# Optimization experiments

Measured on AMD Instinct MI355X. Metric: run time of the kernel, lower is better.

## Reference

```python
import jax, jax.numpy as jnp
from jax import lax
import numpy as np

VGG_C = 512
INNER = 32


def _conv3x3(x, w, b):
    # x: [B,C,H,W], w: [O,I,3,3], padding=1 (SAME)
    y = lax.conv_general_dilated(x, w, (1, 1), 'SAME',
                                 dimension_numbers=('NCHW', 'OIHW', 'NCHW'))
    return y + b[None, :, None, None]


def _predict_filter(style, cw, cb, fw, fb):
    # FilterPredictor_S: conv 512->32, global mean pool, FC 32 -> 9*32*32
    s = _conv3x3(style, cw, cb)                     # [B,32,H,W]
    pooled = s.mean(axis=(2, 3))                    # [B,32]
    f = pooled @ fw.T + fb                          # [B,9216]
    return f.reshape(-1, INNER, INNER, 3, 3)        # [B,outC,inC,3,3]


def _apply_filter(x, filt):
    # per-sample dynamic 3x3 conv: x [B,32,H,W], filt [B,32,32,3,3]
    def one(xi, wi):
        return lax.conv_general_dilated(xi[None], wi, (1, 1), 'SAME',
                                        dimension_numbers=('NCHW', 'OIHW', 'NCHW'))[0]
    return jax.vmap(one)(x, filt)


def setup_inputs() -> dict:
    key = jax.random.key(0)
    ks = jax.random.split(key, 16)
    B, H, W = 8, 64, 64
    sc = 0.02
    d = {
        'content': jax.random.normal(ks[0], (B, VGG_C, H, W), jnp.float32),
        'style': jax.random.normal(ks[1], (B, VGG_C, H, W), jnp.float32),
        'ds_w': jax.random.normal(ks[2], (INNER, VGG_C, 3, 3), jnp.float32) * sc,
        'ds_b': jnp.zeros((INNER,), jnp.float32),
        'up_w': jax.random.normal(ks[3], (VGG_C, INNER, 3, 3), jnp.float32) * sc,
        'up_b': jnp.zeros((VGG_C,), jnp.float32),
        'f1_cw': jax.random.normal(ks[4], (INNER, VGG_C, 3, 3), jnp.float32) * sc,
        'f1_cb': jnp.zeros((INNER,), jnp.float32),
        'f1_fw': jax.random.normal(ks[5], (9 * INNER * INNER, INNER), jnp.float32) * sc,
        'f1_fb': jnp.zeros((9 * INNER * INNER,), jnp.float32),
        'f2_cw': jax.random.normal(ks[6], (INNER, VGG_C, 3, 3), jnp.float32) * sc,
        'f2_cb': jnp.zeros((INNER,), jnp.float32),
        'f2_fw': jax.random.normal(ks[7], (9 * INNER * INNER, INNER), jnp.float32) * sc,
        'f2_fb': jnp.zeros((9 * INNER * INNER,), jnp.float32),
    }
    return d


def reference(content, style, ds_w, ds_b, up_w, up_b,
              f1_cw, f1_cb, f1_fw, f1_fb,
              f2_cw, f2_cb, f2_fw, f2_fb):
    c = _conv3x3(content, ds_w, ds_b)                       # [B,32,H,W]
    filt1 = _predict_filter(style, f1_cw, f1_cb, f1_fw, f1_fb)
    c = _apply_filter(c, filt1)
    c = jnp.where(c >= 0, c, 0.2 * c)                       # LeakyReLU(0.2)
    filt2 = _predict_filter(style, f2_cw, f2_cb, f2_fw, f2_fb)
    c = _apply_filter(c, filt2)
    return content + _conv3x3(c, up_w, up_b)
```

## Files before the change

kernel.cpp:

```cpp
#include <hip/hip_runtime.h>
#include <hip/hip_bf16.h>

#define NB 8
#define NC 512
#define HW 4096
#define INNER 32

typedef unsigned short u16;
typedef unsigned int u32;
typedef __attribute__((ext_vector_type(8))) short bf16x8;
typedef __attribute__((ext_vector_type(4))) float f32x4;

__device__ __forceinline__ float b2f(u16 u) {
    union { u32 a; float f; } z;
    z.a = ((u32)u) << 16;
    return z.f;
}

__device__ __forceinline__ u16 f2b(float v) {
    u32 x = __float_as_uint(v);
    return (u16)((x + 0x7fffu + ((x >> 16) & 1u)) >> 16);
}

__device__ __forceinline__ float ldin(const void* p, int idx, int isf32) {
    if (isf32) return ((const float*)p)[idx];
    return b2f(((const u16*)p)[idx]);
}

__device__ __forceinline__ void gld_lds16(const void* g, void* l) {
    __builtin_amdgcn_global_load_lds(
        (const __attribute__((address_space(1))) unsigned int*)g,
        (__attribute__((address_space(3))) unsigned int*)l, 16, 0, 0);
}

__device__ __forceinline__ int resolve_isf32(int hisf, const void* content) {
    if (hisf >= 0) return hisf;
    int lane = threadIdx.x & 63;
    u16 u = ((const u16*)content)[lane * 2048];
    int e = (u >> 7) & 0xff;
    unsigned long long m = __ballot(e >= 100 && e <= 150);
    return (__popcll(m) < 32) ? 1 : 0;
}


__device__ __forceinline__ void role_style(int bc, const void* style,
        const void* cw1, const void* cw2, float* pooled_raw,
        int isf32, float* smf) {
    int b = bc >> 9, c = bc & 511;
    int base = bc * HW;
    int tid = threadIdx.x;
    float t = 0.f, top = 0.f, bot = 0.f, lft = 0.f, rgt = 0.f;
    if (isf32) {
        const float4* sp = (const float4*)((const float*)style + base);
#pragma unroll
        for (int k = 0; k < 4; k++) {
            int q = tid + k * 256;
            float4 v = sp[q];
            float s4 = (v.x + v.y) + (v.z + v.w);
            int h = q >> 4, w0 = (q & 15) * 4;
            t += s4;
            if (h == 0)   top += s4;
            if (h == 63)  bot += s4;
            if (w0 == 0)  lft += v.x;
            if (w0 == 60) rgt += v.w;
        }
    } else {
        const uint4* sp = (const uint4*)((const u16*)style + base);
#pragma unroll
        for (int k = 0; k < 2; k++) {
            int q = tid + k * 256;
            uint4 v = sp[q];
            float e0 = b2f((u16)(v.x & 0xffffu)), e1 = b2f((u16)(v.x >> 16));
            float e2 = b2f((u16)(v.y & 0xffffu)), e3 = b2f((u16)(v.y >> 16));
            float e4 = b2f((u16)(v.z & 0xffffu)), e5 = b2f((u16)(v.z >> 16));
            float e6 = b2f((u16)(v.w & 0xffffu)), e7 = b2f((u16)(v.w >> 16));
            float s8 = ((e0 + e1) + (e2 + e3)) + ((e4 + e5) + (e6 + e7));
            int h = q >> 3, w0 = (q & 7) * 8;
            t += s8;
            if (h == 0)   top += s8;
            if (h == 63)  bot += s8;
            if (w0 == 0)  lft += e0;
            if (w0 == 56) rgt += e7;
        }
    }
#pragma unroll
    for (int off = 32; off > 0; off >>= 1) {
        t   += __shfl_down(t, off);
        top += __shfl_down(top, off);
        bot += __shfl_down(bot, off);
        lft += __shfl_down(lft, off);
        rgt += __shfl_down(rgt, off);
    }
    int wave = tid >> 6;
    if ((tid & 63) == 0) {
        smf[20 + wave * 5 + 0] = t;   smf[20 + wave * 5 + 1] = top;
        smf[20 + wave * 5 + 2] = bot; smf[20 + wave * 5 + 3] = lft;
        smf[20 + wave * 5 + 4] = rgt;
    }
    __syncthreads();
    if (tid == 0) {
        t   = smf[20] + smf[25] + smf[30] + smf[35];
        top = smf[21] + smf[26] + smf[31] + smf[36];
        bot = smf[22] + smf[27] + smf[32] + smf[37];
        lft = smf[23] + smf[28] + smf[33] + smf[38];
        rgt = smf[24] + smf[29] + smf[34] + smf[39];
        float c00 = ldin(style, base + 0,    isf32);
        float c0W = ldin(style, base + 63,   isf32);
        float cH0 = ldin(style, base + 4032, isf32);
        float cHW = ldin(style, base + 4095, isf32);
        smf[0] = t - bot - rgt + cHW;
        smf[1] = t - bot;
        smf[2] = t - bot - lft + cH0;
        smf[3] = t - rgt;
        smf[4] = t;
        smf[5] = t - lft;
        smf[6] = t - top - rgt + c0W;
        smf[7] = t - top;
        smf[8] = t - top - lft + c00;
    }
    __syncthreads();
    if (tid < 64) {
        int set = tid >> 5, o = tid & 31;
        const void* cw = set ? cw2 : cw1;
        int wb = (o * NC + c) * 9;
        float acc = 0.f;
#pragma unroll
        for (int k = 0; k < 9; k++) acc += ldin(cw, wb + k, isf32) * smf[k];
        atomicAdd(&pooled_raw[(set * NB + b) * 32 + o], acc);
    }
}

__device__ __forceinline__ void role_transform(int ridx, const void* content,
        u16* cT, int bstart, int isf32, float* lds) {
    int hp = ridx & 31;
    int ci = (ridx >> 5) & 15;
    int b4 = ridx >> 9;
    int tid = threadIdx.x;
    size_t gbase = ((size_t)(bstart + b4) * NC + ci * 32) * HW + (size_t)hp * 128;
    if (isf32) {
#pragma unroll
        for (int r2 = 0; r2 < 2; r2++)
#pragma unroll
            for (int k = 0; k < 2; k++) {
                int q = tid + k * 256;
                int c = q >> 4, w0 = (q & 15) * 4;
                float4 v = *(const float4*)((const float*)content
                            + gbase + (size_t)c * HW + r2 * 64 + w0);
                float* dst = lds + r2 * 2080 + c * 65 + w0;
                dst[0] = v.x; dst[1] = v.y; dst[2] = v.z; dst[3] = v.w;
            }
    } else {
#pragma unroll
        for (int r2 = 0; r2 < 2; r2++) {
            int c = tid >> 3, w0 = (tid & 7) * 8;
            uint4 v = *(const uint4*)((const u16*)content
                        + gbase + (size_t)c * HW + r2 * 64 + w0);
            float* dst = lds + r2 * 2080 + c * 65 + w0;
            dst[0] = b2f((u16)(v.x & 0xffffu));
            dst[1] = b2f((u16)(v.x >> 16));
            dst[2] = b2f((u16)(v.y & 0xffffu));
            dst[3] = b2f((u16)(v.y >> 16));
            dst[4] = b2f((u16)(v.z & 0xffffu));
            dst[5] = b2f((u16)(v.z >> 16));
            dst[6] = b2f((u16)(v.w & 0xffffu));
            dst[7] = b2f((u16)(v.w >> 16));
        }
    }
    __syncthreads();
#pragma unroll
    for (int r2 = 0; r2 < 2; r2++) {
        u32* out = (u32*)(cT + ((size_t)(b4 * 16 + ci) * 4096
                                + (hp * 2 + r2) * 64) * 32);
        const float* src = lds + r2 * 2080;
#pragma unroll
        for (int k = 0; k < 4; k++) {
            int j = tid + k * 256;
            int w = j >> 4, cpair = j & 15;
            int key = (w + 1) & 3;
            int p0 = cpair << 1;
            int lc = (((p0 >> 3) ^ key) << 3) | (p0 & 7);
            out[j] = (u32)f2b(src[lc * 65 + w])
                   | ((u32)f2b(src[(lc + 1) * 65 + w]) << 16);
        }
    }
}

__device__ __forceinline__ void role_prep_wdown(int ridx, const void* dsw,
        u16* Bp, int isf32) {
    int idx = ridx * 256 + threadIdx.x;
    int e = idx & 7, l = (idx >> 3) & 63, nf = (idx >> 9) & 1;
    int cb = (idx >> 10) & 15, t9 = idx >> 14;
    int oc = nf * 16 + (l & 15);
    int c = cb * 32 + (l >> 4) * 8 + e;
    Bp[idx] = f2b(ldin(dsw, (oc * NC + c) * 9 + t9, isf32));
}

__device__ __forceinline__ void role_prep_wup(int ridx, const void* upw,
        u16* B2p, int isf32) {
    int idx = ridx * 256 + threadIdx.x;
    int e = idx & 7, l = (idx >> 3) & 63, nfo = (idx >> 9) & 31, t9 = idx >> 14;
    int oc = nfo * 16 + (l & 15);
    int ic = (l >> 4) * 8 + e;
    B2p[idx] = f2b(ldin(upw, (oc * INNER + ic) * 9 + t9, isf32));
}

__device__ __forceinline__ void role_fc(int ridx, const float* pooled_raw,
        const void* cbf1, const void* cbf2,
        const void* fw1, const void* fb1, const void* fw2, const void* fb2,
        u16* fpack, int isf32, float* p) {
    int set = ridx / 288;
    int rr = ridx - set * 288;
    int b = rr / 36;
    int chunk = rr - b * 36;
    int row = chunk * 256 + threadIdx.x;
    const void* fw = set ? fw2 : fw1;
    const void* fb = set ? fb2 : fb1;
    if (threadIdx.x < 32)
        p[threadIdx.x] = pooled_raw[(set * NB + b) * 32 + threadIdx.x]
                           * (1.0f / 4096.0f)
                       + ldin(set ? cbf2 : cbf1, threadIdx.x, isf32);
    __syncthreads();
    float acc = ldin(fb, row, isf32);
    if (isf32) {
        const float* fwf = (const float*)fw + row * 32;
#pragma unroll
        for (int j = 0; j < 32; j++) acc += fwf[j] * p[j];
    } else {
        const u32* w32 = (const u32*)((const u16*)fw + row * 32);
#pragma unroll
        for (int j = 0; j < 16; j++) {
            u32 u = w32[j];
            acc += b2f((u16)(u & 0xffffu)) * p[2 * j];
            acc += b2f((u16)(u >> 16)) * p[2 * j + 1];
        }
    }
    int oc = row / 288;
    int rem = row - oc * 288;
    int ic = rem / 9;
    int t9 = rem - ic * 9;
    int l = (oc & 15) | ((ic >> 3) << 4);
    int e = ic & 7;
    int nf = oc >> 4;
    fpack[((((set * NB + b) * 9 + t9) * 2 + nf) * 64 + l) * 8 + e] = f2b(acc);
}

__device__ __forceinline__ void role_conv_down(int x, const u16* cT,
        const u16* Bp, const void* dsb, u16* c0T, int bstart, int isf32,
        u16* lds) {
    u32* lds32 = (u32*)lds;
    int b4 = x >> 6, row = x & 63;
    int b = bstart + b4;
    int tid = threadIdx.x, lane = tid & 63;
    int wid = __builtin_amdgcn_readfirstlane(tid >> 6);
    for (int i = tid; i < 3 * 66 * 16; i += 256) lds32[i] = 0u;
    __syncthreads();

    int m = lane & 15, g = lane >> 4;
    int wbase = wid * 16;
    f32x4 acc0 = {0.f, 0.f, 0.f, 0.f}, acc1 = {0.f, 0.f, 0.f, 0.f};

    for (int ci = 0; ci < 16; ci++) {
        if (ci) __syncthreads();
        const u16* sp = cT + ((size_t)(b4 * 16 + ci) * 4096) * 32;
#pragma unroll
        for (int r = 0; r < 3; r++) {
            int gh = row + r - 1;
            if (gh >= 0 && gh < 64)
                gld_lds16(sp + (size_t)gh * 2048 + tid * 8,
                          (char*)lds + (r * 66 + 1) * 64 + wid * 1024);
        }
        __syncthreads();
#pragma unroll
        for (int t9 = 0; t9 < 9; t9++) {
            int dh = t9 / 3, dw = t9 - dh * 3;
            int wi = wbase + m + dw;
            bf16x8 a = *(const bf16x8*)(lds + ((dh * 66 + wi) * 32 + ((g ^ (wi & 3)) * 8)));
            bf16x8 b0 = ((const bf16x8*)Bp)[((t9 * 16 + ci) * 2 + 0) * 64 + lane];
            bf16x8 b1 = ((const bf16x8*)Bp)[((t9 * 16 + ci) * 2 + 1) * 64 + lane];
            acc0 = __builtin_amdgcn_mfma_f32_16x16x32_bf16(a, b0, acc0, 0, 0, 0);
            acc1 = __builtin_amdgcn_mfma_f32_16x16x32_bf16(a, b1, acc1, 0, 0, 0);
        }
    }
    float bia0 = ldin(dsb, m, isf32);
    float bia1 = ldin(dsb, 16 + m, isf32);
    size_t obase = ((size_t)b * 4096 + row * 64) * 32;
    int pix0 = wbase + g * 4;
#pragma unroll
    for (int r = 0; r < 4; r++) {
        int w = pix0 + r;
        int key = (w + 1) & 3;
        int p0 = (((m >> 3) ^ key) << 3) | (m & 7);
        int p1 = ((((16 + m) >> 3) ^ key) << 3) | (m & 7);
        c0T[obase + (size_t)w * 32 + p0] = f2b(acc0[r] + bia0);
        c0T[obase + (size_t)w * 32 + p1] = f2b(acc1[r] + bia1);
    }
}


__global__ __launch_bounds__(256) void k_front(
        const void* __restrict__ style,
        const void* __restrict__ cw1, const void* __restrict__ cw2,
        float* __restrict__ pooled_raw, int nStyle,
        const void* __restrict__ content, u16* __restrict__ cT, int bstart, int nT,
        const void* __restrict__ dsw, u16* __restrict__ Bp,
        const void* __restrict__ upw, u16* __restrict__ B2p, int nPrep,
        int hisf) {
    __shared__ float smf[2 * 2080];
    int isf32 = resolve_isf32(hisf, content);
    int x = blockIdx.x;
    if (x < nStyle) { role_style(x, style, cw1, cw2, pooled_raw, isf32, smf); return; }
    x -= nStyle;
    if (x < nT) { role_transform(x, content, cT, bstart, isf32, smf); return; }
    x -= nT;
    if (x < nPrep) { role_prep_wdown(x, dsw, Bp, isf32); return; }
    x -= nPrep;
    role_prep_wup(x, upw, B2p, isf32);
}

__global__ __launch_bounds__(256) void k_mid(
        const u16* __restrict__ cT, const u16* __restrict__ Bp,
        const void* __restrict__ dsb, u16* __restrict__ c0T, int bstart, int nCD,
        const float* __restrict__ pooled_raw,
        const void* __restrict__ cbf1, const void* __restrict__ cbf2,
        const void* __restrict__ fw1, const void* __restrict__ fb1,
        const void* __restrict__ fw2, const void* __restrict__ fb2,
        u16* __restrict__ fpack, const void* __restrict__ content, int hisf) {
    __shared__ u16 lds[3 * 66 * 32];
    int isf32 = resolve_isf32(hisf, content);
    int x = blockIdx.x;
    if (x < nCD) { role_conv_down(x, cT, Bp, dsb, c0T, bstart, isf32, lds); return; }
    role_fc(x - nCD, pooled_raw, cbf1, cbf2, fw1, fb1, fw2, fb2, fpack,
            isf32, (float*)lds);
}

__global__ __launch_bounds__(256) void k_apply(const u16* __restrict__ srcT,
        const u16* __restrict__ fpack, u16* __restrict__ dstT, int lrelu) {
    int b = blockIdx.x >> 6, row = blockIdx.x & 63;
    int tid = threadIdx.x, lane = tid & 63;
    int wid = __builtin_amdgcn_readfirstlane(tid >> 6);
    __shared__ u16 lds[3 * 66 * 32];
    u32* lds32 = (u32*)lds;
    for (int i = tid; i < 96; i += 256) {
        int r = i >> 5, side = (i >> 4) & 1, cpr = i & 15;
        lds32[(r * 66 + side * 65) * 16 + cpr] = 0u;
    }
    const u16* sp = srcT + (size_t)b * 64 * 64 * 32;
    for (int r = 0; r < 3; r++) {
        int gh = row + r - 1;
        u32 ldsoff = (u32)(r * 66 + 1) * 64 + (u32)wid * 1024;
        if (gh >= 0 && gh < 64) {
            gld_lds16(sp + (size_t)gh * 2048 + tid * 8, (char*)lds + ldsoff);
        } else {
            int4 z = make_int4(0, 0, 0, 0);
            *(int4*)((char*)lds + ldsoff + (u32)lane * 16) = z;
        }
    }
    __syncthreads();

    int m = lane & 15, g = lane >> 4, wbase = wid * 16;
    f32x4 acc0 = {0.f, 0.f, 0.f, 0.f}, acc1 = {0.f, 0.f, 0.f, 0.f};
    const bf16x8* FB = (const bf16x8*)fpack + (size_t)b * 1152;
#pragma unroll
    for (int t9 = 0; t9 < 9; t9++) {
        int dh = t9 / 3, dw = t9 - dh * 3;
        int wi = wbase + m + dw;
        bf16x8 a = *(const bf16x8*)(lds + ((dh * 66 + wi) * 32 + ((g ^ (wi & 3)) * 8)));
        bf16x8 b0 = FB[(t9 * 2 + 0) * 64 + lane];
        bf16x8 b1 = FB[(t9 * 2 + 1) * 64 + lane];
        acc0 = __builtin_amdgcn_mfma_f32_16x16x32_bf16(a, b0, acc0, 0, 0, 0);
        acc1 = __builtin_amdgcn_mfma_f32_16x16x32_bf16(a, b1, acc1, 0, 0, 0);
    }
    size_t obase = ((size_t)(b * 64 + row) * 64) * 32;
    int pix0 = wbase + g * 4;
#pragma unroll
    for (int r = 0; r < 4; r++) {
        float v0 = acc0[r], v1 = acc1[r];
        if (lrelu) {
            v0 = (v0 >= 0.f) ? v0 : 0.2f * v0;
            v1 = (v1 >= 0.f) ? v1 : 0.2f * v1;
        }
        int w = pix0 + r;
        int key = (w + 1) & 3;
        int p0 = (((m >> 3) ^ key) << 3) | (m & 7);
        int p1 = ((((16 + m) >> 3) ^ key) << 3) | (m & 7);
        dstT[obase + (size_t)w * 32 + p0] = f2b(v0);
        dstT[obase + (size_t)w * 32 + p1] = f2b(v1);
    }
}

__global__ __launch_bounds__(256) void k_conv_up(const u16* __restrict__ c2T,
        const u16* __restrict__ B2p, const void* __restrict__ upb,
        const void* __restrict__ content, void* __restrict__ outv, int hisf) {
    int isf32 = resolve_isf32(hisf, content);
    int b = blockIdx.x >> 6, row = blockIdx.x & 63;
    int nq = blockIdx.y;
    int tid = threadIdx.x, lane = tid & 63;
    int wid = __builtin_amdgcn_readfirstlane(tid >> 6);
    __shared__ char smem[64 * 68 * 4] __attribute__((aligned(16)));
    u16* lds = (u16*)smem;
    u32* lds32 = (u32*)smem;
    for (int i = tid; i < 96; i += 256) {
        int r = i >> 5, side = (i >> 4) & 1, cpr = i & 15;
        lds32[(r * 66 + side * 65) * 16 + cpr] = 0u;
    }
    const u16* sp = c2T + (size_t)b * 64 * 64 * 32;
    for (int r = 0; r < 3; r++) {
        int gh = row + r - 1;
        u32 ldsoff = (u32)(r * 66 + 1) * 64 + (u32)wid * 1024;
        if (gh >= 0 && gh < 64) {
            gld_lds16(sp + (size_t)gh * 2048 + tid * 8, (char*)lds + ldsoff);
        } else {
            int4 z = make_int4(0, 0, 0, 0);
            *(int4*)((char*)lds + ldsoff + (u32)lane * 16) = z;
        }
    }
    __syncthreads();

    int m = lane & 15, g = lane >> 4, wbase = wid * 16;
    f32x4 acc[8];
#pragma unroll
    for (int i = 0; i < 8; i++) acc[i] = (f32x4){0.f, 0.f, 0.f, 0.f};
#pragma unroll
    for (int t9 = 0; t9 < 9; t9++) {
        int dh = t9 / 3, dw = t9 - dh * 3;
        int wi = wbase + m + dw;
        bf16x8 a = *(const bf16x8*)(lds + ((dh * 66 + wi) * 32 + ((g ^ (wi & 3)) * 8)));
#pragma unroll
        for (int nfl = 0; nfl < 8; nfl++) {
            bf16x8 bw = ((const bf16x8*)B2p)[(t9 * 32 + nq * 8 + nfl) * 64 + lane];
            acc[nfl] = __builtin_amdgcn_mfma_f32_16x16x32_bf16(a, bw, acc[nfl], 0, 0, 0);
        }
    }

    int pix0 = wbase + g * 4;
    float* fl = (float*)smem;
    int ocl2 = tid >> 4;
    int px0 = (tid & 15) * 4;
    __syncthreads();
#pragma unroll
    for (int hf = 0; hf < 2; hf++) {
        if (hf) __syncthreads();
#pragma unroll
        for (int nf = 0; nf < 4; nf++) {
            int ocl = nf * 16 + m;
            *(f32x4*)(fl + ocl * 68 + pix0) = acc[hf * 4 + nf];
        }
        __syncthreads();
#pragma unroll
        for (int p = 0; p < 4; p++) {
            int ocl = p * 16 + ocl2;
            int oc = nq * 128 + hf * 64 + ocl;
            float bias = ldin(upb, oc, isf32);
            f32x4 v4 = *(const f32x4*)(fl + ocl * 68 + px0);
            size_t idx = ((size_t)b * NC + oc) * HW + (size_t)row * 64 + px0;
            if (isf32) {
                f32x4 rsd = *(const f32x4*)((const float*)content + idx);
                f32x4 ov;
#pragma unroll
                for (int r = 0; r < 4; r++) ov[r] = v4[r] + bias + rsd[r];
                *(f32x4*)((float*)outv + idx) = ov;
            } else {
                ushort4 rv = *(const ushort4*)((const u16*)content + idx);
                ushort4 ov;
                ov.x = f2b(v4[0] + bias + b2f(rv.x));
                ov.y = f2b(v4[1] + bias + b2f(rv.y));
                ov.z = f2b(v4[2] + bias + b2f(rv.z));
                ov.w = f2b(v4[3] + bias + b2f(rv.w));
                *(ushort4*)((u16*)outv + idx) = ov;
            }
        }
    }
}

extern "C" void kernel_launch(void* const* d_in, const int* in_sizes, int n_in,
                              void* d_out, int out_size, void* d_ws, size_t ws_size,
                              hipStream_t stream) {
    const void* content = d_in[0];
    const void* style   = d_in[1];
    const void* ds_w    = d_in[2];
    const void* ds_b    = d_in[3];
    const void* up_w    = d_in[4];
    const void* up_b    = d_in[5];
    const void* f1_cw   = d_in[6];
    const void* f1_cb   = d_in[7];
    const void* f1_fw   = d_in[8];
    const void* f1_fb   = d_in[9];
    const void* f2_cw   = d_in[10];
    const void* f2_cb   = d_in[11];
    const void* f2_fw   = d_in[12];
    const void* f2_fb   = d_in[13];

    int hisf = -1;
    if (in_sizes && n_in >= 1) {
        if (in_sizes[0] == NB * NC * HW * 4) hisf = 1;
        else if (in_sizes[0] == NB * NC * HW * 2) hisf = 0;
    }

    const size_t SZ_PACK = 294912;
    const size_t SZ_CT2  = 2097152;
    const size_t REQ_WS  = 3 * SZ_CT2 + 3 * SZ_PACK + 2048 + 64;

    if (ws_size >= REQ_WS) {
        char* w = (char*)d_ws;
        u16*   B2pack = (u16*)w;                 w += SZ_PACK;
        u16*   c2T    = (u16*)w;                 w += SZ_CT2;
        u16*   c0T    = (u16*)w;                 w += SZ_CT2;
        u16*   c1T    = (u16*)w;                 w += SZ_CT2;
        u16*   Bpack  = (u16*)w;                 w += SZ_PACK;
        u16*   fpack  = (u16*)w;                 w += SZ_PACK;
        float* pooled_raw = (float*)w;
        u16*   cT     = (u16*)d_out;

        hipMemsetAsync(pooled_raw, 0, 2 * NB * 32 * 4, stream);
        k_front<<<4096 + 4096 + 2 * 576, 256, 0, stream>>>(
            style, f1_cw, f2_cw, pooled_raw, 4096,
            content, cT, 0, 4096,
            ds_w, Bpack, up_w, B2pack, 576, hisf);
        k_mid<<<512 + 576, 256, 0, stream>>>(
            cT, Bpack, ds_b, c0T, 0, 512,
            pooled_raw, f1_cb, f2_cb,
            f1_fw, f1_fb, f2_fw, f2_fb, fpack, content, hisf);
        k_apply<<<NB * 64, 256, 0, stream>>>(c0T, fpack, c1T, 1);
        k_apply<<<NB * 64, 256, 0, stream>>>(c1T, fpack + NB * 9216, c2T, 0);
        k_conv_up<<<dim3(NB * 64, 4), 256, 0, stream>>>(c2T, B2pack, up_b,
                                                        content, d_out, hisf);
    } else {
        float* pooled_raw = (float*)d_out;
        u16*   fpack  = (u16*)(pooled_raw + 512);
        u16*   Bpack  = fpack + 147456;
        u16*   c0T    = Bpack + 147456;
        u16*   c1T    = c0T + 1048576;
        u16*   cTh    = c1T + 1048576;
        u16*   B2pack = (u16*)d_ws;
        u16*   c2T    = B2pack + 147456;

        hipMemsetAsync(pooled_raw, 0, 2 * NB * 32 * 4, stream);
        k_front<<<4096 + 2048 + 2 * 576, 256, 0, stream>>>(
            style, f1_cw, f2_cw, pooled_raw, 4096,
            content, cTh, 0, 2048,
            ds_w, Bpack, up_w, B2pack, 576, hisf);
        k_mid<<<256 + 576, 256, 0, stream>>>(
            cTh, Bpack, ds_b, c0T, 0, 256,
            pooled_raw, f1_cb, f2_cb,
            f1_fw, f1_fb, f2_fw, f2_fb, fpack, content, hisf);
        k_front<<<2048, 256, 0, stream>>>(
            style, f1_cw, f2_cw, pooled_raw, 0,
            content, cTh, 4, 2048,
            ds_w, Bpack, up_w, B2pack, 0, hisf);
        k_mid<<<256, 256, 0, stream>>>(
            cTh, Bpack, ds_b, c0T, 4, 256,
            pooled_raw, f1_cb, f2_cb,
            f1_fw, f1_fb, f2_fw, f2_fb, fpack, content, hisf);
        k_apply<<<NB * 64, 256, 0, stream>>>(c0T, fpack, c1T, 1);
        k_apply<<<NB * 64, 256, 0, stream>>>(c1T, fpack + NB * 9216, c2T, 0);
        k_conv_up<<<dim3(NB * 64, 4), 256, 0, stream>>>(c2T, B2pack, up_b,
                                                        content, d_out, hisf);
    }
}
```

Measured before the change: 283.7 us.

## Move style/transform roles to per-wave work and split output channels across waves

The style-reduction and content-transpose roles now run one work item per wave instead of per block. This removes block-level syncthreads and shared-memory reductions, and the grid shrinks by four. The conv-down, filter-apply and filter-predict kernels move to 512-thread blocks in which each wave computes one 16-channel output half instead of two, so each wave keeps a single accumulator. This adds occupancy and wave-level parallelism, at the cost of redundant A-fragment LDS reads and larger blocks.

After: 282.3 us. About the same (-0.5%).

```diff
diff --git a/kernel.cpp b/kernel.cpp
--- a/kernel.cpp
+++ b/kernel.cpp
@@ -43,145 +43,122 @@
 }
 
 
-__device__ __forceinline__ void role_style(int bc, const void* style,
-        const void* cw1, const void* cw2, float* pooled_raw,
-        int isf32, float* smf) {
+__device__ __forceinline__ void role_style_wave(int bc, const void* style,
+        const void* cw1, const void* cw2, float* pooled_raw, int isf32) {
     int b = bc >> 9, c = bc & 511;
     int base = bc * HW;
-    int tid = threadIdx.x;
+    int lane = threadIdx.x & 63;
     float t = 0.f, top = 0.f, bot = 0.f, lft = 0.f, rgt = 0.f;
     if (isf32) {
         const float4* sp = (const float4*)((const float*)style + base);
 #pragma unroll
-        for (int k = 0; k < 4; k++) {
-            int q = tid + k * 256;
-            float4 v = sp[q];
+        for (int k = 0; k < 16; k++) {
+            float4 v = sp[lane + 64 * k];
             float s4 = (v.x + v.y) + (v.z + v.w);
-            int h = q >> 4, w0 = (q & 15) * 4;
             t += s4;
-            if (h == 0)   top += s4;
-            if (h == 63)  bot += s4;
-            if (w0 == 0)  lft += v.x;
-            if (w0 == 60) rgt += v.w;
+            if (k == 0  && lane < 16)  top += s4;
+            if (k == 15 && lane >= 48) bot += s4;
+            if ((lane & 15) == 0)  lft += v.x;
+            if ((lane & 15) == 15) rgt += v.w;
         }
     } else {
         const uint4* sp = (const uint4*)((const u16*)style + base);
 #pragma unroll
-        for (int k = 0; k < 2; k++) {
-            int q = tid + k * 256;
-            uint4 v = sp[q];
+        for (int k = 0; k < 8; k++) {
+            uint4 v = sp[lane + 64 * k];
             float e0 = b2f((u16)(v.x & 0xffffu)), e1 = b2f((u16)(v.x >> 16));
             float e2 = b2f((u16)(v.y & 0xffffu)), e3 = b2f((u16)(v.y >> 16));
             float e4 = b2f((u16)(v.z & 0xffffu)), e5 = b2f((u16)(v.z >> 16));
             float e6 = b2f((u16)(v.w & 0xffffu)), e7 = b2f((u16)(v.w >> 16));
             float s8 = ((e0 + e1) + (e2 + e3)) + ((e4 + e5) + (e6 + e7));
-            int h = q >> 3, w0 = (q & 7) * 8;
             t += s8;
-            if (h == 0)   top += s8;
-            if (h == 63)  bot += s8;
-            if (w0 == 0)  lft += e0;
-            if (w0 == 56) rgt += e7;
-        }
-    }
-#pragma unroll
-    for (int off = 32; off > 0; off >>= 1) {
-        t   += __shfl_down(t, off);
-        top += __shfl_down(top, off);
-        bot += __shfl_down(bot, off);
-        lft += __shfl_down(lft, off);
-        rgt += __shfl_down(rgt, off);
-    }
-    int wave = tid >> 6;
-    if ((tid & 63) == 0) {
-        smf[20 + wave * 5 + 0] = t;   smf[20 + wave * 5 + 1] = top;
-        smf[20 + wave * 5 + 2] = bot; smf[20 + wave * 5 + 3] = lft;
-        smf[20 + wave * 5 + 4] = rgt;
-    }
-    __syncthreads();
-    if (tid == 0) {
-        t   = smf[20] + smf[25] + smf[30] + smf[35];
-        top = smf[21] + smf[26] + smf[31] + smf[36];
-        bot = smf[22] + smf[27] + smf[32] + smf[37];
-        lft = smf[23] + smf[28] + smf[33] + smf[38];
-        rgt = smf[24] + smf[29] + smf[34] + smf[39];
-        float c00 = ldin(style, base + 0,    isf32);
-        float c0W = ldin(style, base + 63,   isf32);
-        float cH0 = ldin(style, base + 4032, isf32);
-        float cHW = ldin(style, base + 4095, isf32);
-        smf[0] = t - bot - rgt + cHW;
-        smf[1] = t - bot;
-        smf[2] = t - bot - lft + cH0;
-        smf[3] = t - rgt;
-        smf[4] = t;
-        smf[5] = t - lft;
-        smf[6] = t - top - rgt + c0W;
-        smf[7] = t - top;
-        smf[8] = t - top - lft + c00;
-    }
-    __syncthreads();
-    if (tid < 64) {
-        int set = tid >> 5, o = tid & 31;
-        const void* cw = set ? cw2 : cw1;
-        int wb = (o * NC + c) * 9;
-        float acc = 0.f;
-#pragma unroll
-        for (int k = 0; k < 9; k++) acc += ldin(cw, wb + k, isf32) * smf[k];
-        atomicAdd(&pooled_raw[(set * NB + b) * 32 + o], acc);
-    }
-}
-
-__device__ __forceinline__ void role_transform(int ridx, const void* content,
-        u16* cT, int bstart, int isf32, float* lds) {
-    int hp = ridx & 31;
-    int ci = (ridx >> 5) & 15;
-    int b4 = ridx >> 9;
-    int tid = threadIdx.x;
-    size_t gbase = ((size_t)(bstart + b4) * NC + ci * 32) * HW + (size_t)hp * 128;
-    if (isf32) {
-#pragma unroll
-        for (int r2 = 0; r2 < 2; r2++)
-#pragma unroll
-            for (int k = 0; k < 2; k++) {
-                int q = tid + k * 256;
-                int c = q >> 4, w0 = (q & 15) * 4;
-                float4 v = *(const float4*)((const float*)content
-                            + gbase + (size_t)c * HW + r2 * 64 + w0);
-                float* dst = lds + r2 * 2080 + c * 65 + w0;
-                dst[0] = v.x; dst[1] = v.y; dst[2] = v.z; dst[3] = v.w;
+            if (k == 0 && lane < 8)   top += s8;
+            if (k == 7 && lane >= 56) bot += s8;
+            if ((lane & 7) == 0) lft += e0;
+            if ((lane & 7) == 7) rgt += e7;
+        }
+    }
+#pragma unroll
+    for (int off = 1; off < 64; off <<= 1) {
+        t   += __shfl_xor(t, off);
+        top += __shfl_xor(top, off);
+        bot += __shfl_xor(bot, off);
+        lft += __shfl_xor(lft, off);
+        rgt += __shfl_xor(rgt, off);
+    }
+    float c00 = ldin(style, base + 0,    isf32);
+    float c0W = ldin(style, base + 63,   isf32);
+    float cH0 = ldin(style, base + 4032, isf32);
+    float cHW = ldin(style, base + 4095, isf32);
+    float s[9];
+    s[0] = t - bot - rgt + cHW;
+    s[1] = t - bot;
+    s[2] = t - bot - lft + cH0;
+    s[3] = t - rgt;
+    s[4] = t;
+    s[5] = t - lft;
+    s[6] = t - top - rgt + c0W;
+    s[7] = t - top;
+    s[8] = t - top - lft + c00;
+    int set = lane >> 5, o = lane & 31;
+    const void* cw = set ? cw2 : cw1;
+    int wb = (o * NC + c) * 9;
+    float acc = 0.f;
+#pragma unroll
+    for (int k = 0; k < 9; k++) acc += ldin(cw, wb + k, isf32) * s[k];
+    atomicAdd(&pooled_raw[(set * NB + b) * 32 + o], acc);
+}
+
+__device__ __forceinline__ void role_transform_wave(int ridx,
+        const void* content, u16* cT, int bstart, int isf32,
+        u16* wl ) {
+    int hq = ridx & 15;
+    int ci = (ridx >> 4) & 15;
+    int b4 = ridx >> 8;
+    int lane = threadIdx.x & 63;
+    size_t pbase = ((size_t)(bstart + b4) * NC + ci * 32) * HW;
+    int c  = lane >> 1;
+    int w0 = (lane & 1) * 32;
+    int wq = lane >> 2;
+    int cq = (lane & 3) * 4;
+
+    for (int i = 0; i < 4; i++) {
+        int h = hq * 4 + i;
+        if (isf32) {
+            const float* src = (const float*)content + pbase
+                               + (size_t)c * HW + h * 64 + w0;
+#pragma unroll
+            for (int j = 0; j < 8; j++) {
+                float4 v = *(const float4*)(src + j * 4);
+                u32 lo = (u32)f2b(v.x) | ((u32)f2b(v.y) << 16);
+                u32 hi = (u32)f2b(v.z) | ((u32)f2b(v.w) << 16);
+                *(uint2*)(wl + c * 72 + w0 + j * 4) = make_uint2(lo, hi);
             }
-    } else {
-#pragma unroll
-        for (int r2 = 0; r2 < 2; r2++) {
-            int c = tid >> 3, w0 = (tid & 7) * 8;
-            uint4 v = *(const uint4*)((const u16*)content
-                        + gbase + (size_t)c * HW + r2 * 64 + w0);
-            float* dst = lds + r2 * 2080 + c * 65 + w0;
-            dst[0] = b2f((u16)(v.x & 0xffffu));
-            dst[1] = b2f((u16)(v.x >> 16));
-            dst[2] = b2f((u16)(v.y & 0xffffu));
-            dst[3] = b2f((u16)(v.y >> 16));
-            dst[4] = b2f((u16)(v.z & 0xffffu));
-            dst[5] = b2f((u16)(v.z >> 16));
-            dst[6] = b2f((u16)(v.w & 0xffffu));
-            dst[7] = b2f((u16)(v.w >> 16));
-        }
-    }
-    __syncthreads();
-#pragma unroll
-    for (int r2 = 0; r2 < 2; r2++) {
-        u32* out = (u32*)(cT + ((size_t)(b4 * 16 + ci) * 4096
-                                + (hp * 2 + r2) * 64) * 32);
-        const float* src = lds + r2 * 2080;
+        } else {
+            const u16* src = (const u16*)content + pbase
+                             + (size_t)c * HW + h * 64 + w0;
+#pragma unroll
+            for (int j = 0; j < 4; j++) {
+                uint4 v = *(const uint4*)(src + j * 8);
+                *(uint4*)(wl + c * 72 + w0 + j * 8) = v;
+            }
+        }
+        asm volatile("s_waitcnt lgkmcnt(0)" ::: "memory");
+        u32* out = (u32*)(cT + (((size_t)(b4 * 16 + ci)) * 4096 + h * 64) * 32);
 #pragma unroll
         for (int k = 0; k < 4; k++) {
-            int j = tid + k * 256;
-            int w = j >> 4, cpair = j & 15;
+            int w = wq + 16 * k;
             int key = (w + 1) & 3;
-            int p0 = cpair << 1;
-            int lc = (((p0 >> 3) ^ key) << 3) | (p0 & 7);
-            out[j] = (u32)f2b(src[lc * 65 + w])
-                   | ((u32)f2b(src[(lc + 1) * 65 + w]) << 16);
-        }
+            u32 q[4];
+#pragma unroll
+            for (int e = 0; e < 4; e++) {
+                int p0 = 2 * (cq + e);
+                int lc = (((p0 >> 3) ^ key) << 3) | (p0 & 7);
+                q[e] = (u32)wl[lc * 72 + w] | ((u32)wl[(lc + 1) * 72 + w] << 16);
+            }
+            *(uint4*)(out + k * 256 + lane * 4) = make_uint4(q[0], q[1], q[2], q[3]);
+        }
+        asm volatile("s_waitcnt lgkmcnt(0)" ::: "memory");
     }
 }
 
@@ -208,11 +185,11 @@
         const void* cbf1, const void* cbf2,
         const void* fw1, const void* fb1, const void* fw2, const void* fb2,
         u16* fpack, int isf32, float* p) {
-    int set = ridx / 288;
-    int rr = ridx - set * 288;
-    int b = rr / 36;
-    int chunk = rr - b * 36;
-    int row = chunk * 256 + threadIdx.x;
+    int set = ridx / 144;
+    int rr = ridx - set * 144;
+    int b = rr / 18;
+    int chunk = rr - b * 18;
+    int row = chunk * 512 + threadIdx.x;
     const void* fw = set ? fw2 : fw1;
     const void* fb = set ? fb2 : fb1;
     if (threadIdx.x < 32)
@@ -252,22 +229,23 @@
     int b = bstart + b4;
     int tid = threadIdx.x, lane = tid & 63;
     int wid = __builtin_amdgcn_readfirstlane(tid >> 6);
-    for (int i = tid; i < 3 * 66 * 16; i += 256) lds32[i] = 0u;
+    for (int i = tid; i < 3 * 66 * 16; i += 512) lds32[i] = 0u;
     __syncthreads();
 
     int m = lane & 15, g = lane >> 4;
-    int wbase = wid * 16;
-    f32x4 acc0 = {0.f, 0.f, 0.f, 0.f}, acc1 = {0.f, 0.f, 0.f, 0.f};
+    int wq = wid & 3, ocf = wid >> 2;
+    int wbase = wq * 16;
+    int sr = wid >> 1, sh = wid & 1;
+    f32x4 acc = {0.f, 0.f, 0.f, 0.f};
 
     for (int ci = 0; ci < 16; ci++) {
         if (ci) __syncthreads();
         const u16* sp = cT + ((size_t)(b4 * 16 + ci) * 4096) * 32;
-#pragma unroll
-        for (int r = 0; r < 3; r++) {
-            int gh = row + r - 1;
+        if (wid < 6) {
+            int gh = row + sr - 1;
             if (gh >= 0 && gh < 64)
-                gld_lds16(sp + (size_t)gh * 2048 + tid * 8,
-                          (char*)lds + (r * 66 + 1) * 64 + wid * 1024);
+                gld_lds16(sp + (size_t)gh * 2048 + (sh * 64 + lane) * 8,
+                          (char*)lds + (sr * 66 + 1) * 64 + sh * 1024);
         }
         __syncthreads();
 #pragma unroll
@@ -275,24 +253,20 @@
             int dh = t9 / 3, dw = t9 - dh * 3;
             int wi = wbase + m + dw;
             bf16x8 a = *(const bf16x8*)(lds + ((dh * 66 + wi) * 32 + ((g ^ (wi & 3)) * 8)));
-            bf16x8 b0 = ((const bf16x8*)Bp)[((t9 * 16 + ci) * 2 + 0) * 64 + lane];
-            bf16x8 b1 = ((const bf16x8*)Bp)[((t9 * 16 + ci) * 2 + 1) * 64 + lane];
-            acc0 = __builtin_amdgcn_mfma_f32_16x16x32_bf16(a, b0, acc0, 0, 0, 0);
-            acc1 = __builtin_amdgcn_mfma_f32_16x16x32_bf16(a, b1, acc1, 0, 0, 0);
-        }
-    }
-    float bia0 = ldin(dsb, m, isf32);
-    float bia1 = ldin(dsb, 16 + m, isf32);
+            bf16x8 bb = ((const bf16x8*)Bp)[((t9 * 16 + ci) * 2 + ocf) * 64 + lane];
+            acc = __builtin_amdgcn_mfma_f32_16x16x32_bf16(a, bb, acc, 0, 0, 0);
+        }
+    }
+    int oc = ocf * 16 + m;
+    float bia = ldin(dsb, oc, isf32);
     size_t obase = ((size_t)b * 4096 + row * 64) * 32;
     int pix0 = wbase + g * 4;
 #pragma unroll
     for (int r = 0; r < 4; r++) {
         int w = pix0 + r;
         int key = (w + 1) & 3;
-        int p0 = (((m >> 3) ^ key) << 3) | (m & 7);
-        int p1 = ((((16 + m) >> 3) ^ key) << 3) | (m & 7);
-        c0T[obase + (size_t)w * 32 + p0] = f2b(acc0[r] + bia0);
-        c0T[obase + (size_t)w * 32 + p1] = f2b(acc1[r] + bia1);
+        int p = (((oc >> 3) ^ key) << 3) | (oc & 7);
+        c0T[obase + (size_t)w * 32 + p] = f2b(acc[r] + bia);
     }
 }
 
@@ -300,24 +274,31 @@
 __global__ __launch_bounds__(256) void k_front(
         const void* __restrict__ style,
         const void* __restrict__ cw1, const void* __restrict__ cw2,
-        float* __restrict__ pooled_raw, int nStyle,
-        const void* __restrict__ content, u16* __restrict__ cT, int bstart, int nT,
+        float* __restrict__ pooled_raw, int nStyleB,
+        const void* __restrict__ content, u16* __restrict__ cT, int bstart, int nTB,
         const void* __restrict__ dsw, u16* __restrict__ Bp,
         const void* __restrict__ upw, u16* __restrict__ B2p, int nPrep,
         int hisf) {
-    __shared__ float smf[2 * 2080];
+    __shared__ u16 smT[4][2304];
     int isf32 = resolve_isf32(hisf, content);
+    int wid = threadIdx.x >> 6;
     int x = blockIdx.x;
-    if (x < nStyle) { role_style(x, style, cw1, cw2, pooled_raw, isf32, smf); return; }
-    x -= nStyle;
-    if (x < nT) { role_transform(x, content, cT, bstart, isf32, smf); return; }
-    x -= nT;
+    if (x < nStyleB) {
+        role_style_wave(x * 4 + wid, style, cw1, cw2, pooled_raw, isf32);
+        return;
+    }
+    x -= nStyleB;
+    if (x < nTB) {
+        role_transform_wave(x * 4 + wid, content, cT, bstart, isf32, smT[wid]);
+        return;
+    }
+    x -= nTB;
     if (x < nPrep) { role_prep_wdown(x, dsw, Bp, isf32); return; }
     x -= nPrep;
     role_prep_wup(x, upw, B2p, isf32);
 }
 
-__global__ __launch_bounds__(256) void k_mid(
+__global__ __launch_bounds__(512) void k_mid(
         const u16* __restrict__ cT, const u16* __restrict__ Bp,
         const void* __restrict__ dsb, u16* __restrict__ c0T, int bstart, int nCD,
         const float* __restrict__ pooled_raw,
@@ -333,23 +314,25 @@
             isf32, (float*)lds);
 }
 
-__global__ __launch_bounds__(256) void k_apply(const u16* __restrict__ srcT,
+__global__ __launch_bounds__(512) void k_apply(const u16* __restrict__ srcT,
         const u16* __restrict__ fpack, u16* __restrict__ dstT, int lrelu) {
     int b = blockIdx.x >> 6, row = blockIdx.x & 63;
     int tid = threadIdx.x, lane = tid & 63;
     int wid = __builtin_amdgcn_readfirstlane(tid >> 6);
     __shared__ u16 lds[3 * 66 * 32];
     u32* lds32 = (u32*)lds;
-    for (int i = tid; i < 96; i += 256) {
+    for (int i = tid; i < 96; i += 512) {
         int r = i >> 5, side = (i >> 4) & 1, cpr = i & 15;
         lds32[(r * 66 + side * 65) * 16 + cpr] = 0u;
     }
     const u16* sp = srcT + (size_t)b * 64 * 64 * 32;
-    for (int r = 0; r < 3; r++) {
-        int gh = row + r - 1;
-        u32 ldsoff = (u32)(r * 66 + 1) * 64 + (u32)wid * 1024;
+    if (wid < 6) {
+        int sr = wid >> 1, sh = wid & 1;
+        int gh = row + sr - 1;
+        u32 ldsoff = (u32)(sr * 66 + 1) * 64 + (u32)sh * 1024;
         if (gh >= 0 && gh < 64) {
-            gld_lds16(sp + (size_t)gh * 2048 + tid * 8, (char*)lds + ldsoff);
+            gld_lds16(sp + (size_t)gh * 2048 + (sh * 64 + lane) * 8,
+                      (char*)lds + ldsoff);
         } else {
             int4 z = make_int4(0, 0, 0, 0);
             *(int4*)((char*)lds + ldsoff + (u32)lane * 16) = z;
@@ -357,34 +340,30 @@
     }
     __syncthreads();
 
-    int m = lane & 15, g = lane >> 4, wbase = wid * 16;
-    f32x4 acc0 = {0.f, 0.f, 0.f, 0.f}, acc1 = {0.f, 0.f, 0.f, 0.f};
+    int m = lane & 15, g = lane >> 4;
+    int wq = wid & 3, ocf = wid >> 2;
+    int wbase = wq * 16;
+    f32x4 acc = {0.f, 0.f, 0.f, 0.f};
     const bf16x8* FB = (const bf16x8*)fpack + (size_t)b * 1152;
 #pragma unroll
     for (int t9 = 0; t9 < 9; t9++) {
         int dh = t9 / 3, dw = t9 - dh * 3;
         int wi = wbase + m + dw;
         bf16x8 a = *(const bf16x8*)(lds + ((dh * 66 + wi) * 32 + ((g ^ (wi & 3)) * 8)));
-        bf16x8 b0 = FB[(t9 * 2 + 0) * 64 + lane];
-        bf16x8 b1 = FB[(t9 * 2 + 1) * 64 + lane];
-        acc0 = __builtin_amdgcn_mfma_f32_16x16x32_bf16(a, b0, acc0, 0, 0, 0);
-        acc1 = __builtin_amdgcn_mfma_f32_16x16x32_bf16(a, b1, acc1, 0, 0, 0);
-    }
+        bf16x8 bb = FB[(t9 * 2 + ocf) * 64 + lane];
+        acc = __builtin_amdgcn_mfma_f32_16x16x32_bf16(a, bb, acc, 0, 0, 0);
+    }
+    int oc = ocf * 16 + m;
     size_t obase = ((size_t)(b * 64 + row) * 64) * 32;
     int pix0 = wbase + g * 4;
 #pragma unroll
     for (int r = 0; r < 4; r++) {
-        float v0 = acc0[r], v1 = acc1[r];
-        if (lrelu) {
-            v0 = (v0 >= 0.f) ? v0 : 0.2f * v0;
-            v1 = (v1 >= 0.f) ? v1 : 0.2f * v1;
-        }
+        float v = acc[r];
+        if (lrelu) v = (v >= 0.f) ? v : 0.2f * v;
         int w = pix0 + r;
         int key = (w + 1) & 3;
-        int p0 = (((m >> 3) ^ key) << 3) | (m & 7);
-        int p1 = ((((16 + m) >> 3) ^ key) << 3) | (m & 7);
-        dstT[obase + (size_t)w * 32 + p0] = f2b(v0);
-        dstT[obase + (size_t)w * 32 + p1] = f2b(v1);
+        int p = (((oc >> 3) ^ key) << 3) | (oc & 7);
+        dstT[obase + (size_t)w * 32 + p] = f2b(v);
     }
 }
 
@@ -512,16 +491,16 @@
         u16*   cT     = (u16*)d_out;
 
         hipMemsetAsync(pooled_raw, 0, 2 * NB * 32 * 4, stream);
-        k_front<<<4096 + 4096 + 2 * 576, 256, 0, stream>>>(
-            style, f1_cw, f2_cw, pooled_raw, 4096,
-            content, cT, 0, 4096,
+        k_front<<<1024 + 512 + 2 * 576, 256, 0, stream>>>(
+            style, f1_cw, f2_cw, pooled_raw, 1024,
+            content, cT, 0, 512,
             ds_w, Bpack, up_w, B2pack, 576, hisf);
-        k_mid<<<512 + 576, 256, 0, stream>>>(
+        k_mid<<<512 + 288, 512, 0, stream>>>(
             cT, Bpack, ds_b, c0T, 0, 512,
             pooled_raw, f1_cb, f2_cb,
             f1_fw, f1_fb, f2_fw, f2_fb, fpack, content, hisf);
-        k_apply<<<NB * 64, 256, 0, stream>>>(c0T, fpack, c1T, 1);
-        k_apply<<<NB * 64, 256, 0, stream>>>(c1T, fpack + NB * 9216, c2T, 0);
+        k_apply<<<NB * 64, 512, 0, stream>>>(c0T, fpack, c1T, 1);
+        k_apply<<<NB * 64, 512, 0, stream>>>(c1T, fpack + NB * 9216, c2T, 0);
         k_conv_up<<<dim3(NB * 64, 4), 256, 0, stream>>>(c2T, B2pack, up_b,
                                                         content, d_out, hisf);
     } else {
@@ -535,24 +514,24 @@
         u16*   c2T    = B2pack + 147456;
 
         hipMemsetAsync(pooled_raw, 0, 2 * NB * 32 * 4, stream);
-        k_front<<<4096 + 2048 + 2 * 576, 256, 0, stream>>>(
-            style, f1_cw, f2_cw, pooled_raw, 4096,
-            content, cTh, 0, 2048,
+        k_front<<<1024 + 256 + 2 * 576, 256, 0, stream>>>(
+            style, f1_cw, f2_cw, pooled_raw, 1024,
+            content, cTh, 0, 256,
             ds_w, Bpack, up_w, B2pack, 576, hisf);
-        k_mid<<<256 + 576, 256, 0, stream>>>(
+        k_mid<<<256 + 288, 512, 0, stream>>>(
             cTh, Bpack, ds_b, c0T, 0, 256,
             pooled_raw, f1_cb, f2_cb,
             f1_fw, f1_fb, f2_fw, f2_fb, fpack, content, hisf);
-        k_front<<<2048, 256, 0, stream>>>(
+        k_front<<<256, 256, 0, stream>>>(
             style, f1_cw, f2_cw, pooled_raw, 0,
-            content, cTh, 4, 2048,
+            content, cTh, 4, 256,
             ds_w, Bpack, up_w, B2pack, 0, hisf);
-        k_mid<<<256, 256, 0, stream>>>(
+        k_mid<<<256, 512, 0, stream>>>(
             cTh, Bpack, ds_b, c0T, 4, 256,
             pooled_raw, f1_cb, f2_cb,
             f1_fw, f1_fb, f2_fw, f2_fb, fpack, content, hisf);
-        k_apply<<<NB * 64, 256, 0, stream>>>(c0T, fpack, c1T, 1);
-        k_apply<<<NB * 64, 256, 0, stream>>>(c1T, fpack + NB * 9216, c2T, 0);
+        k_apply<<<NB * 64, 512, 0, stream>>>(c0T, fpack, c1T, 1);
+        k_apply<<<NB * 64, 512, 0, stream>>>(c1T, fpack + NB * 9216, c2T, 0);
         k_conv_up<<<dim3(NB * 64, 4), 256, 0, stream>>>(c2T, B2pack, up_b,
                                                         content, d_out, hisf);
     }
```
